# Kernel tuning notes

Hardware: AMD Instinct MI355X
Metric: run time of the kernel (lower is better)

The kernel has to match this reference:

```python
import jax, jax.numpy as jnp
import numpy as np

B, L, D = 4, 4096, 128
WINDOW = 64
NEG = -1e9
LN_EPS = 1e-5


def setup_inputs() -> dict:
    key = jax.random.key(0)
    ks = jax.random.split(key, 6)
    x = jax.random.normal(ks[0], (B, L, D), dtype=jnp.float32)
    # windowed adjacency with self-loops: adj[b,i,j]=1 iff |i-j| <= WINDOW
    idx = jnp.arange(L)
    band = (jnp.abs(idx[:, None] - idx[None, :]) <= WINDOW).astype(jnp.int32)
    adj = jnp.broadcast_to(band, (B, L, L))
    mask = np.ones((B, L), dtype=np.int32)
    mask[B // 2 :, -L // 8 :] = 0
    mask = jnp.asarray(mask)
    s = 1.0 / np.sqrt(D)
    Wq = jax.random.normal(ks[1], (D, D), dtype=jnp.float32) * s
    Wk = jax.random.normal(ks[2], (D, D), dtype=jnp.float32) * s
    Wv = jax.random.normal(ks[3], (D, D), dtype=jnp.float32) * s
    W_upd = jax.random.normal(ks[4], (2 * D, D), dtype=jnp.float32) * (1.0 / np.sqrt(2 * D))
    b_upd = jnp.zeros((D,), dtype=jnp.float32)
    gamma = jnp.ones((D,), dtype=jnp.float32)
    beta = jnp.zeros((D,), dtype=jnp.float32)
    return {"x": x, "adj": adj, "mask": mask, "Wq": Wq, "Wk": Wk, "Wv": Wv,
            "W_upd": W_upd, "b_upd": b_upd, "gamma": gamma, "beta": beta}


def reference(x, adj, mask, Wq, Wk, Wv, W_upd, b_upd, gamma, beta):
    d = x.shape[-1]
    q = jnp.einsum("bld,de->ble", x, Wq)
    k = jnp.einsum("bld,de->ble", x, Wk)
    v = jnp.einsum("bld,de->ble", x, Wv)
    logits = jnp.einsum("bld,bmd->blm", q, k) / jnp.sqrt(jnp.float32(d))
    logits = jnp.where(adj == 0, NEG, logits)
    logits = jnp.where(mask[:, :, None] == 0, NEG, logits)
    logits = jnp.where(mask[:, None, :] == 0, NEG, logits)
    attn = jax.nn.softmax(logits, axis=-1)  # dropout = identity (eval mode)
    agg = jnp.einsum("blm,bmd->bld", attn, v)
    h = jnp.concatenate([x, agg], axis=-1)  # [B, L, 2D]
    upd = jax.nn.relu(h @ W_upd + b_upd)
    y = x + upd
    mu = jnp.mean(y, axis=-1, keepdims=True)
    var = jnp.var(y, axis=-1, keepdims=True)
    return gamma * (y - mu) * jax.lax.rsqrt(var + LN_EPS) + beta
```

## Files before the change

kernel.cpp:

```cpp
#include <hip/hip_runtime.h>

#define BB 4
#define LL 4096
#define DD 128
#define WIN 64
#define BL (BB * LL)

typedef unsigned short u16;

__device__ __forceinline__ u16 f2b(float f) {
  union { float f; unsigned int u; } x;
  x.f = f;
  unsigned int r = x.u + 0x7fffu + ((x.u >> 16) & 1u);
  return (u16)(r >> 16);
}
__device__ __forceinline__ float b2f_lo(unsigned int u) {
  union { unsigned int u; float f; } x;
  x.u = u << 16;
  return x.f;
}
__device__ __forceinline__ float b2f_hi(unsigned int u) {
  union { unsigned int u; float f; } x;
  x.u = u & 0xffff0000u;
  return x.f;
}
__device__ __forceinline__ void unpack8(uint4 u, float* f) {
  f[0] = b2f_lo(u.x); f[1] = b2f_hi(u.x);
  f[2] = b2f_lo(u.y); f[3] = b2f_hi(u.y);
  f[4] = b2f_lo(u.z); f[5] = b2f_hi(u.z);
  f[6] = b2f_lo(u.w); f[7] = b2f_hi(u.w);
}
__device__ __forceinline__ float comp4(float4 a, int d) {
  return d == 0 ? a.x : (d == 1 ? a.y : (d == 2 ? a.z : a.w));
}

__global__ __launch_bounds__(256) void qkv_kernel(
    const float* __restrict__ x, const float* __restrict__ Wq,
    const float* __restrict__ Wk, const float* __restrict__ Wv,
    u16* __restrict__ q, u16* __restrict__ k, u16* __restrict__ v,
    float* __restrict__ vmean_sum) {
  __shared__ float xs[64][132];

  const int t = threadIdx.x;
  const int row0 = blockIdx.x * 64;
  const int which = blockIdx.y;
  const float* __restrict__ W = which == 0 ? Wq : (which == 1 ? Wk : Wv);
  u16* __restrict__ outp = which == 0 ? q : (which == 1 ? k : v);

  {
    const float4* xg = (const float4*)(x + (size_t)row0 * DD);
    #pragma unroll
    for (int p = 0; p < 8; ++p) {
      int idx = t + 256 * p;
      ((float4*)&xs[idx >> 5][0])[idx & 31] = xg[idx];
    }
  }
  __syncthreads();

  const int rg = t >> 5;
  const int cg = t & 31;
  const float4* W4 = (const float4*)W;

  float4 acc[8];
  #pragma unroll
  for (int m = 0; m < 8; ++m) acc[m] = make_float4(0.f, 0.f, 0.f, 0.f);

  #pragma unroll 2
  for (int k4 = 0; k4 < 32; ++k4) {
    float4 a[8];
    #pragma unroll
    for (int m = 0; m < 8; ++m)
      a[m] = ((const float4*)&xs[rg + 8 * m][0])[k4];
    #pragma unroll
    for (int d = 0; d < 4; ++d) {
      float4 w = W4[(size_t)(k4 * 4 + d) * 32 + cg];
      #pragma unroll
      for (int m = 0; m < 8; ++m) {
        float av = comp4(a[m], d);
        acc[m].x += av * w.x; acc[m].y += av * w.y;
        acc[m].z += av * w.z; acc[m].w += av * w.w;
      }
    }
  }

  #pragma unroll
  for (int m = 0; m < 8; ++m) {
    ushort4 s;
    s.x = f2b(acc[m].x); s.y = f2b(acc[m].y);
    s.z = f2b(acc[m].z); s.w = f2b(acc[m].w);
    *(ushort4*)(outp + (size_t)(row0 + rg + 8 * m) * DD + 4 * cg) = s;
  }

  if (which == 2) {
    __syncthreads();
    float4 cs = make_float4(0.f, 0.f, 0.f, 0.f);
    #pragma unroll
    for (int m = 0; m < 8; ++m) {
      cs.x += acc[m].x; cs.y += acc[m].y; cs.z += acc[m].z; cs.w += acc[m].w;
    }
    ((float4*)&xs[rg][0])[cg] = cs;
    __syncthreads();
    if (t < DD) {
      float s = 0.f;
      #pragma unroll
      for (int r = 0; r < 8; ++r) s += xs[r][t];
      atomicAdd(&vmean_sum[(row0 >> 12) * DD + t], s);
    }
  }
}

struct SMemA {
  u16 qs[32][136];
  u16 ks[64][136];
  u16 vs[64][136];
  float pt[64][36];
  int cms[64];
  float rowsum[32];
};
struct SMemM {
  float hs[32][264];
};
union SMemU {
  SMemA a;
  SMemM m;
};

__global__ __launch_bounds__(256) void attn_mlp_kernel(
    const u16* __restrict__ q, const u16* __restrict__ k,
    const u16* __restrict__ v, const float* __restrict__ vmean_sum,
    const int* __restrict__ mask, const float* __restrict__ x,
    const float* __restrict__ Wu, const float* __restrict__ bias,
    const float* __restrict__ gamma, const float* __restrict__ beta,
    float* __restrict__ out) {
  __shared__ __align__(16) SMemU sm;

  const int bx = blockIdx.x;
  const int b = bx >> 7;
  const int i0 = (bx & 127) * 32;
  const int t = threadIdx.x;
  const int tm = t >> 4;
  const int tn = t & 15;
  const size_t rowbase = ((size_t)b * LL + i0) * DD;

  {
    const uint4* qg = (const uint4*)(q + rowbase);
    #pragma unroll
    for (int p = 0; p < 2; ++p) {
      int idx = t + 256 * p;
      *(uint4*)&sm.a.qs[idx >> 4][8 * (idx & 15)] = qg[idx];
    }
  }

  float accv[2][8];
  float lsum[2];
  #pragma unroll
  for (int r = 0; r < 2; ++r) {
    lsum[r] = 0.f;
    #pragma unroll
    for (int j = 0; j < 8; ++j) accv[r][j] = 0.f;
  }

  for (int ch = 0; ch < 3; ++ch) {
    const int j0 = i0 - WIN + ch * 64;
    __syncthreads();

    {
      const uint4* kg = (const uint4*)(k + (size_t)b * LL * DD);
      const uint4* vg = (const uint4*)(v + (size_t)b * LL * DD);
      #pragma unroll
      for (int p = 0; p < 4; ++p) {
        int idx = t + 256 * p;
        int row = idx >> 4, c = idx & 15;
        int j = j0 + row;
        int jc = j < 0 ? 0 : (j > LL - 1 ? LL - 1 : j);
        *(uint4*)&sm.a.ks[row][8 * c] = kg[(size_t)jc * 16 + c];
        *(uint4*)&sm.a.vs[row][8 * c] = vg[(size_t)jc * 16 + c];
      }
      if (t < 64) {
        int j = j0 + t;
        sm.a.cms[t] = (j >= 0 && j < LL) ? mask[b * LL + j] : 0;
      }
    }
    __syncthreads();

    float S[2][4];
    #pragma unroll
    for (int m = 0; m < 2; ++m)
      #pragma unroll
      for (int n = 0; n < 4; ++n) S[m][n] = 0.f;

    for (int k8 = 0; k8 < 16; ++k8) {
      float af[2][8], bf[4][8];
      #pragma unroll
      for (int m = 0; m < 2; ++m)
        unpack8(*(const uint4*)&sm.a.qs[tm + 16 * m][8 * k8], af[m]);
      #pragma unroll
      for (int n = 0; n < 4; ++n)
        unpack8(*(const uint4*)&sm.a.ks[tn + 16 * n][8 * k8], bf[n]);
      #pragma unroll
      for (int m = 0; m < 2; ++m)
        #pragma unroll
        for (int n = 0; n < 4; ++n) {
          float s = S[m][n];
          #pragma unroll
          for (int j = 0; j < 8; ++j) s += af[m][j] * bf[n][j];
          S[m][n] = s;
        }
    }

    #pragma unroll
    for (int m = 0; m < 2; ++m) {
      int row = tm + 16 * m;
      int iR = i0 + row;
      #pragma unroll
      for (int n = 0; n < 4; ++n) {
        int col = tn + 16 * n;
        int j = j0 + col;
        int dj = iR - j;
        dj = dj < 0 ? -dj : dj;
        bool ok =
            (dj <= WIN) && ((unsigned)j < (unsigned)LL) && (sm.a.cms[col] != 0);
        float p = ok ? __expf(S[m][n] * 0.08838834764831845f) : 0.f;
        lsum[m] += p;
        sm.a.pt[col][row] = p;
      }
    }
    __syncthreads();

    #pragma unroll 2
    for (int c = 0; c < 64; ++c) {
      float2 pv = *(const float2*)&sm.a.pt[c][2 * tm];
      float vf[8];
      unpack8(*(const uint4*)&sm.a.vs[c][8 * tn], vf);
      #pragma unroll
      for (int j = 0; j < 8; ++j) {
        accv[0][j] += pv.x * vf[j];
        accv[1][j] += pv.y * vf[j];
      }
    }
  }

  #pragma unroll
  for (int m = 0; m < 2; ++m) {
    float l = lsum[m];
    l += __shfl_xor(l, 1);
    l += __shfl_xor(l, 2);
    l += __shfl_xor(l, 4);
    l += __shfl_xor(l, 8);
    if (tn == 0) sm.a.rowsum[tm + 16 * m] = l;
  }
  __syncthreads();

  #pragma unroll
  for (int r = 0; r < 2; ++r) {
    int row = 2 * tm + r;
    float inv = 1.0f / sm.a.rowsum[row];
    float o[8];
    if (mask[b * LL + i0 + row] != 0) {
      #pragma unroll
      for (int j = 0; j < 8; ++j) o[j] = accv[r][j] * inv;
    } else {
      const float s = 1.0f / LL;
      #pragma unroll
      for (int j = 0; j < 8; ++j) o[j] = vmean_sum[b * DD + 8 * tn + j] * s;
    }
    *(float4*)&sm.m.hs[row][128 + 8 * tn] = make_float4(o[0], o[1], o[2], o[3]);
    *(float4*)&sm.m.hs[row][132 + 8 * tn] = make_float4(o[4], o[5], o[6], o[7]);
  }
  {
    const float4* xg = (const float4*)(x + rowbase);
    #pragma unroll
    for (int p = 0; p < 4; ++p) {
      int idx = t + 256 * p;
      int row = idx >> 5, c4 = idx & 31;
      ((float4*)&sm.m.hs[row][0])[c4] = xg[row * 32 + c4];
    }
  }
  __syncthreads();

  const int rg = t >> 5;
  const int cg = t & 31;
  float4 acc[4];
  #pragma unroll
  for (int m = 0; m < 4; ++m) acc[m] = make_float4(0.f, 0.f, 0.f, 0.f);
  const float4* Wu4 = (const float4*)Wu;

  #pragma unroll 2
  for (int k4 = 0; k4 < 64; ++k4) {
    float4 a[4];
    #pragma unroll
    for (int m = 0; m < 4; ++m)
      a[m] = ((const float4*)&sm.m.hs[rg + 8 * m][0])[k4];
    #pragma unroll
    for (int d = 0; d < 4; ++d) {
      float4 w = Wu4[(size_t)(k4 * 4 + d) * 32 + cg];
      #pragma unroll
      for (int m = 0; m < 4; ++m) {
        float av = comp4(a[m], d);
        acc[m].x += av * w.x; acc[m].y += av * w.y;
        acc[m].z += av * w.z; acc[m].w += av * w.w;
      }
    }
  }

  const float4 bv = ((const float4*)bias)[cg];
  const float4 g = ((const float4*)gamma)[cg];
  const float4 be = ((const float4*)beta)[cg];

  #pragma unroll
  for (int m = 0; m < 4; ++m) {
    int row = rg + 8 * m;
    float4 xr = ((const float4*)&sm.m.hs[row][0])[cg];
    float y0 = xr.x + fmaxf(acc[m].x + bv.x, 0.f);
    float y1 = xr.y + fmaxf(acc[m].y + bv.y, 0.f);
    float y2 = xr.z + fmaxf(acc[m].z + bv.z, 0.f);
    float y3 = xr.w + fmaxf(acc[m].w + bv.w, 0.f);
    float s = y0 + y1 + y2 + y3;
    float ss = y0 * y0 + y1 * y1 + y2 * y2 + y3 * y3;
    #pragma unroll
    for (int off = 16; off > 0; off >>= 1) {
      s += __shfl_xor(s, off);
      ss += __shfl_xor(ss, off);
    }
    float mu = s * (1.0f / DD);
    float var = ss * (1.0f / DD) - mu * mu;
    float rstd = rsqrtf(var + 1e-5f);
    float4 o = make_float4(g.x * ((y0 - mu) * rstd) + be.x,
                           g.y * ((y1 - mu) * rstd) + be.y,
                           g.z * ((y2 - mu) * rstd) + be.z,
                           g.w * ((y3 - mu) * rstd) + be.w);
    ((float4*)(out + rowbase + (size_t)row * DD))[cg] = o;
  }
}

extern "C" void kernel_launch(void* const* d_in, const int* in_sizes, int n_in,
                              void* d_out, int out_size, void* d_ws,
                              size_t ws_size, hipStream_t stream) {
  const float* x = (const float*)d_in[0];
  const int* mask = (const int*)d_in[2];
  const float* Wq = (const float*)d_in[3];
  const float* Wk = (const float*)d_in[4];
  const float* Wv = (const float*)d_in[5];
  const float* Wu = (const float*)d_in[6];
  const float* bias = (const float*)d_in[7];
  const float* gamma = (const float*)d_in[8];
  const float* beta = (const float*)d_in[9];
  float* out = (float*)d_out;

  u16* q = (u16*)d_ws;
  u16* k = q + (size_t)BL * DD;
  u16* v = k + (size_t)BL * DD;
  float* vmean_sum = (float*)(v + (size_t)BL * DD);

  hipMemsetAsync(vmean_sum, 0, BB * DD * sizeof(float), stream);

  qkv_kernel<<<dim3(BL / 64, 3), 256, 0, stream>>>(x, Wq, Wk, Wv, q, k, v,
                                                   vmean_sum);
  attn_mlp_kernel<<<BL / 32, 256, 0, stream>>>(q, k, v, vmean_sum, mask, x, Wu,
                                               bias, gamma, beta, out);
}
```

Measured before the change: 389.7 us.

## Run update MLP on bf16 MFMA with pre-transposed bf16 weights

The fused attention+MLP kernel's final [32x256]x[256x128] update GEMM moves from scalar fp32 FMAs to bf16 16x16x32 MFMA instructions. The h tile is staged in shared memory as bf16, and W_upd is transposed and converted to bf16 by an extra slice of the qkv launch. The aim is to cut the ALU-bound epilogue GEMM cost. LayerNorm is restructured around a shared fp32 y buffer. The cost is bf16 rounding of x and W_upd in the update path, plus extra grid blocks in the qkv launch.

```diff
diff --git a/kernel.cpp b/kernel.cpp
--- a/kernel.cpp
+++ b/kernel.cpp
@@ -7,6 +7,8 @@
 #define BL (BB * LL)
 
 typedef unsigned short u16;
+using bf16x8 = __attribute__((ext_vector_type(8))) short;
+using f32x4 = __attribute__((ext_vector_type(4))) float;
 
 __device__ __forceinline__ u16 f2b(float f) {
   union { float f; unsigned int u; } x;
@@ -37,13 +39,25 @@
 __global__ __launch_bounds__(256) void qkv_kernel(
     const float* __restrict__ x, const float* __restrict__ Wq,
     const float* __restrict__ Wk, const float* __restrict__ Wv,
-    u16* __restrict__ q, u16* __restrict__ k, u16* __restrict__ v,
-    float* __restrict__ vmean_sum) {
+    const float* __restrict__ Wu, u16* __restrict__ q, u16* __restrict__ k,
+    u16* __restrict__ v, float* __restrict__ vmean_sum,
+    u16* __restrict__ Wut) {
   __shared__ float xs[64][132];
 
   const int t = threadIdx.x;
+  const int which = blockIdx.y;
+
+  if (which == 3) {
+    if (blockIdx.x < 128) {
+      int idx = blockIdx.x * 256 + t;
+      int n = idx >> 8;
+      int kd = idx & 255;
+      Wut[n * 256 + kd] = f2b(Wu[kd * 128 + n]);
+    }
+    return;
+  }
+
   const int row0 = blockIdx.x * 64;
-  const int which = blockIdx.y;
   const float* __restrict__ W = which == 0 ? Wq : (which == 1 ? Wk : Wv);
   u16* __restrict__ outp = which == 0 ? q : (which == 1 ? k : v);
 
@@ -109,30 +123,28 @@
   }
 }
 
-struct SMemA {
+struct SA {
   u16 qs[32][136];
   u16 ks[64][136];
   u16 vs[64][136];
   float pt[64][36];
-  int cms[64];
-  float rowsum[32];
 };
-struct SMemM {
-  float hs[32][264];
+struct SM {
+  u16 hs[32][264];
+  float ys[32][132];
 };
-union SMemU {
-  SMemA a;
-  SMemM m;
-};
+union SU { SA a; SM m; };
 
 __global__ __launch_bounds__(256) void attn_mlp_kernel(
     const u16* __restrict__ q, const u16* __restrict__ k,
     const u16* __restrict__ v, const float* __restrict__ vmean_sum,
     const int* __restrict__ mask, const float* __restrict__ x,
-    const float* __restrict__ Wu, const float* __restrict__ bias,
+    const u16* __restrict__ Wut, const float* __restrict__ bias,
     const float* __restrict__ gamma, const float* __restrict__ beta,
     float* __restrict__ out) {
-  __shared__ __align__(16) SMemU sm;
+  __shared__ __align__(16) SU sm;
+  __shared__ int cms[64];
+  __shared__ float rowsum[32];
 
   const int bx = blockIdx.x;
   const int b = bx >> 7;
@@ -178,7 +190,7 @@
       }
       if (t < 64) {
         int j = j0 + t;
-        sm.a.cms[t] = (j >= 0 && j < LL) ? mask[b * LL + j] : 0;
+        cms[t] = (j >= 0 && j < LL) ? mask[b * LL + j] : 0;
       }
     }
     __syncthreads();
@@ -218,8 +230,7 @@
         int j = j0 + col;
         int dj = iR - j;
         dj = dj < 0 ? -dj : dj;
-        bool ok =
-            (dj <= WIN) && ((unsigned)j < (unsigned)LL) && (sm.a.cms[col] != 0);
+        bool ok = (dj <= WIN) && ((unsigned)j < (unsigned)LL) && (cms[col] != 0);
         float p = ok ? __expf(S[m][n] * 0.08838834764831845f) : 0.f;
         lsum[m] += p;
         sm.a.pt[col][row] = p;
@@ -247,14 +258,14 @@
     l += __shfl_xor(l, 2);
     l += __shfl_xor(l, 4);
     l += __shfl_xor(l, 8);
-    if (tn == 0) sm.a.rowsum[tm + 16 * m] = l;
+    if (tn == 0) rowsum[tm + 16 * m] = l;
   }
   __syncthreads();
 
   #pragma unroll
   for (int r = 0; r < 2; ++r) {
     int row = 2 * tm + r;
-    float inv = 1.0f / sm.a.rowsum[row];
+    float inv = 1.0f / rowsum[row];
     float o[8];
     if (mask[b * LL + i0 + row] != 0) {
       #pragma unroll
@@ -264,8 +275,11 @@
       #pragma unroll
       for (int j = 0; j < 8; ++j) o[j] = vmean_sum[b * DD + 8 * tn + j] * s;
     }
-    *(float4*)&sm.m.hs[row][128 + 8 * tn] = make_float4(o[0], o[1], o[2], o[3]);
-    *(float4*)&sm.m.hs[row][132 + 8 * tn] = make_float4(o[4], o[5], o[6], o[7]);
+    ushort4 pk;
+    pk.x = f2b(o[0]); pk.y = f2b(o[1]); pk.z = f2b(o[2]); pk.w = f2b(o[3]);
+    *(ushort4*)&sm.m.hs[row][DD + 8 * tn] = pk;
+    pk.x = f2b(o[4]); pk.y = f2b(o[5]); pk.z = f2b(o[6]); pk.w = f2b(o[7]);
+    *(ushort4*)&sm.m.hs[row][DD + 8 * tn + 4] = pk;
   }
   {
     const float4* xg = (const float4*)(x + rowbase);
@@ -273,63 +287,87 @@
     for (int p = 0; p < 4; ++p) {
       int idx = t + 256 * p;
       int row = idx >> 5, c4 = idx & 31;
-      ((float4*)&sm.m.hs[row][0])[c4] = xg[row * 32 + c4];
+      float4 xv = xg[row * 32 + c4];
+      ushort4 pk;
+      pk.x = f2b(xv.x); pk.y = f2b(xv.y); pk.z = f2b(xv.z); pk.w = f2b(xv.w);
+      *(ushort4*)&sm.m.hs[row][4 * c4] = pk;
     }
   }
   __syncthreads();
 
-  const int rg = t >> 5;
-  const int cg = t & 31;
-  float4 acc[4];
-  #pragma unroll
-  for (int m = 0; m < 4; ++m) acc[m] = make_float4(0.f, 0.f, 0.f, 0.f);
-  const float4* Wu4 = (const float4*)Wu;
-
+  const int w = t >> 6;
+  const int lane = t & 63;
+  const int quad = lane >> 4;
+  const int l16 = lane & 15;
+  const f32x4 zero4 = {0.f, 0.f, 0.f, 0.f};
+
+  f32x4 upd[2][2];
+  upd[0][0] = zero4; upd[0][1] = zero4;
+  upd[1][0] = zero4; upd[1][1] = zero4;
   #pragma unroll 2
-  for (int k4 = 0; k4 < 64; ++k4) {
-    float4 a[4];
-    #pragma unroll
-    for (int m = 0; m < 4; ++m)
-      a[m] = ((const float4*)&sm.m.hs[rg + 8 * m][0])[k4];
-    #pragma unroll
-    for (int d = 0; d < 4; ++d) {
-      float4 w = Wu4[(size_t)(k4 * 4 + d) * 32 + cg];
-      #pragma unroll
-      for (int m = 0; m < 4; ++m) {
-        float av = comp4(a[m], d);
-        acc[m].x += av * w.x; acc[m].y += av * w.y;
-        acc[m].z += av * w.z; acc[m].w += av * w.w;
-      }
-    }
-  }
-
-  const float4 bv = ((const float4*)bias)[cg];
-  const float4 g = ((const float4*)gamma)[cg];
-  const float4 be = ((const float4*)beta)[cg];
-
-  #pragma unroll
-  for (int m = 0; m < 4; ++m) {
-    int row = rg + 8 * m;
-    float4 xr = ((const float4*)&sm.m.hs[row][0])[cg];
-    float y0 = xr.x + fmaxf(acc[m].x + bv.x, 0.f);
-    float y1 = xr.y + fmaxf(acc[m].y + bv.y, 0.f);
-    float y2 = xr.z + fmaxf(acc[m].z + bv.z, 0.f);
-    float y3 = xr.w + fmaxf(acc[m].w + bv.w, 0.f);
-    float s = y0 + y1 + y2 + y3;
-    float ss = y0 * y0 + y1 * y1 + y2 * y2 + y3 * y3;
-    #pragma unroll
-    for (int off = 16; off > 0; off >>= 1) {
-      s += __shfl_xor(s, off);
-      ss += __shfl_xor(ss, off);
-    }
+  for (int ks8 = 0; ks8 < 8; ++ks8) {
+    bf16x8 ah[2];
+    #pragma unroll
+    for (int mt = 0; mt < 2; ++mt)
+      ah[mt] = *(const bf16x8*)&sm.m.hs[mt * 16 + l16][32 * ks8 + 8 * quad];
+    #pragma unroll
+    for (int ntl = 0; ntl < 2; ++ntl) {
+      int n = (2 * w + ntl) * 16 + l16;
+      bf16x8 bw = *(const bf16x8*)&Wut[(size_t)n * 256 + 32 * ks8 + 8 * quad];
+      #pragma unroll
+      for (int mt = 0; mt < 2; ++mt)
+        upd[mt][ntl] = __builtin_amdgcn_mfma_f32_16x16x32_bf16(
+            ah[mt], bw, upd[mt][ntl], 0, 0, 0);
+    }
+  }
+
+  #pragma unroll
+  for (int mt = 0; mt < 2; ++mt) {
+    #pragma unroll
+    for (int ntl = 0; ntl < 2; ++ntl) {
+      int dim = (2 * w + ntl) * 16 + l16;
+      float bv = bias[dim];
+      #pragma unroll
+      for (int r = 0; r < 4; ++r) {
+        int row = mt * 16 + quad * 4 + r;
+        float u = upd[mt][ntl][r] + bv;
+        u = u > 0.f ? u : 0.f;
+        sm.m.ys[row][dim] = x[rowbase + (size_t)row * DD + dim] + u;
+      }
+    }
+  }
+  __syncthreads();
+
+  {
+    const int row = t >> 3, sg = t & 7;
+    float4 yv[4];
+    float s = 0.f, ss = 0.f;
+    #pragma unroll
+    for (int i = 0; i < 4; ++i) {
+      yv[i] = *(const float4*)&sm.m.ys[row][16 * sg + 4 * i];
+      s += yv[i].x + yv[i].y + yv[i].z + yv[i].w;
+      ss += yv[i].x * yv[i].x + yv[i].y * yv[i].y + yv[i].z * yv[i].z +
+            yv[i].w * yv[i].w;
+    }
+    s += __shfl_xor(s, 1); ss += __shfl_xor(ss, 1);
+    s += __shfl_xor(s, 2); ss += __shfl_xor(ss, 2);
+    s += __shfl_xor(s, 4); ss += __shfl_xor(ss, 4);
     float mu = s * (1.0f / DD);
     float var = ss * (1.0f / DD) - mu * mu;
     float rstd = rsqrtf(var + 1e-5f);
-    float4 o = make_float4(g.x * ((y0 - mu) * rstd) + be.x,
-                           g.y * ((y1 - mu) * rstd) + be.y,
-                           g.z * ((y2 - mu) * rstd) + be.z,
-                           g.w * ((y3 - mu) * rstd) + be.w);
-    ((float4*)(out + rowbase + (size_t)row * DD))[cg] = o;
+    float* op = out + rowbase + (size_t)row * DD;
+    #pragma unroll
+    for (int i = 0; i < 4; ++i) {
+      int d0 = 16 * sg + 4 * i;
+      float4 g = *(const float4*)&gamma[d0];
+      float4 be = *(const float4*)&beta[d0];
+      float4 o;
+      o.x = g.x * ((yv[i].x - mu) * rstd) + be.x;
+      o.y = g.y * ((yv[i].y - mu) * rstd) + be.y;
+      o.z = g.z * ((yv[i].z - mu) * rstd) + be.z;
+      o.w = g.w * ((yv[i].w - mu) * rstd) + be.w;
+      *(float4*)&op[d0] = o;
+    }
   }
 }
 
@@ -351,11 +389,12 @@
   u16* k = q + (size_t)BL * DD;
   u16* v = k + (size_t)BL * DD;
   float* vmean_sum = (float*)(v + (size_t)BL * DD);
+  u16* Wut = (u16*)(vmean_sum + BB * DD);
 
   hipMemsetAsync(vmean_sum, 0, BB * DD * sizeof(float), stream);
 
-  qkv_kernel<<<dim3(BL / 64, 3), 256, 0, stream>>>(x, Wq, Wk, Wv, q, k, v,
-                                                   vmean_sum);
-  attn_mlp_kernel<<<BL / 32, 256, 0, stream>>>(q, k, v, vmean_sum, mask, x, Wu,
-                                               bias, gamma, beta, out);
-}
+  qkv_kernel<<<dim3(BL / 64, 4), 256, 0, stream>>>(x, Wq, Wk, Wv, Wu, q, k, v,
+                                                   vmean_sum, Wut);
+  attn_mlp_kernel<<<BL / 32, 256, 0, stream>>>(q, k, v, vmean_sum, mask, x,
+                                               Wut, bias, gamma, beta, out);
+}
```

Result: no change. 382.8 us (-1.8%).
